# Performance work log

Hardware: AMD Instinct MI355X
Metric: run time of the kernel (lower is better)

## Reference

```python
import jax, jax.numpy as jnp
import numpy as np

NEG_INF = -1e9
LEAKY_SLOPE = 0.2


def setup_inputs() -> dict:
    key = jax.random.key(0)
    k1, k2, k3, k4, k5 = jax.random.split(key, 5)
    B, N, F_in, F_out = 8, 2048, 256, 256
    x = jax.random.normal(k1, (B, N, F_in), dtype=jnp.float32)
    adj = jax.random.randint(k2, (B, N, N), 0, 2, dtype=jnp.int32)
    W = jax.random.normal(k3, (F_out, F_in), dtype=jnp.float32) * 0.05
    a_src = jax.random.normal(k4, (F_out,), dtype=jnp.float32) * 0.05
    a_dst = jax.random.normal(k5, (F_out,), dtype=jnp.float32) * 0.05
    return {"x": x, "adj": adj, "W": W, "a_src": a_src, "a_dst": a_dst}


def reference(x, adj, W, a_src, a_dst):
    # h: (B, N, F_out)
    h = jnp.einsum("bnf,of->bno", x, W)
    # a([h_i ; h_j]) == h_i @ a_src + h_j @ a_dst  (avoids O(N^2, 2F) concat)
    s_src = h @ a_src  # (B, N) score contribution of row node i
    s_dst = h @ a_dst  # (B, N) score contribution of col node j
    e = s_src[:, :, None] + s_dst[:, None, :]  # (B, N, N)
    e = jax.nn.leaky_relu(e, negative_slope=LEAKY_SLOPE)
    e = jnp.where(adj == 0, jnp.float32(NEG_INF), e)
    alpha = jax.nn.softmax(e, axis=-1)  # dropout is identity in eval mode
    h_prime = jnp.einsum("bij,bjo->bio", alpha, h)
    return h_prime
```

## Files before the change

### kernel.cpp

```cpp
#include <hip/hip_runtime.h>
#include <hip/hip_bf16.h>
#include <cstdint>
#include <cstddef>

typedef __attribute__((ext_vector_type(8))) short short8;
typedef __attribute__((ext_vector_type(4))) short short4v;
typedef __attribute__((ext_vector_type(4))) float floatx4;
typedef unsigned short ushort_t;

#define LOG2E 1.44269504088896340736f

__device__ __forceinline__ unsigned short f2bf(float f) {
    unsigned u = __float_as_uint(f);
    u += 0x7FFFu + ((u >> 16) & 1u);
    return (unsigned short)(u >> 16);
}
__device__ __forceinline__ float bf2f(unsigned short s) {
    return __uint_as_float(((unsigned)s) << 16);
}

__global__ __launch_bounds__(256) void wprep(const float* __restrict__ W,
                                             ushort_t* __restrict__ Wb) {
    int t = blockIdx.x * 256 + threadIdx.x;
    float4 v = ((const float4*)W)[t];
    short4v s;
    s[0] = (short)f2bf(v.x); s[1] = (short)f2bf(v.y);
    s[2] = (short)f2bf(v.z); s[3] = (short)f2bf(v.w);
    ((short4v*)Wb)[t] = s;
}

__global__ __launch_bounds__(256) void gemm_h(const float* __restrict__ x,
                                              const ushort_t* __restrict__ Wb,
                                              ushort_t* __restrict__ hT,
                                              const float* __restrict__ a_src,
                                              const float* __restrict__ a_dst,
                                              float* __restrict__ s_src,
                                              float* __restrict__ s_dst) {
    const int tid = threadIdx.x;
    const int w = tid >> 6, lane = tid & 63;
    const int q = lane >> 4, t16 = lane & 15;

    __shared__ ushort_t wt[256][72];

    const int jrow = blockIdx.x * 64 + w * 16 + t16;
    const float* xr = x + (size_t)jrow * 256 + q * 8;
    short8 af[8];
#pragma unroll
    for (int kb = 0; kb < 8; ++kb) {
        float4 v0 = *(const float4*)(xr + kb * 32);
        float4 v1 = *(const float4*)(xr + kb * 32 + 4);
        short8 a;
        a[0] = (short)f2bf(v0.x); a[1] = (short)f2bf(v0.y);
        a[2] = (short)f2bf(v0.z); a[3] = (short)f2bf(v0.w);
        a[4] = (short)f2bf(v1.x); a[5] = (short)f2bf(v1.y);
        a[6] = (short)f2bf(v1.z); a[7] = (short)f2bf(v1.w);
        af[kb] = a;
    }

    floatx4 acc[16] = {};
#pragma unroll
    for (int kp = 0; kp < 4; ++kp) {
        if (kp) __syncthreads();
#pragma unroll
        for (int r = 0; r < 8; ++r) {
            int G = tid + 256 * r;
            int row = G >> 3, g = G & 7;
            int4 wv = *(const int4*)(Wb + (size_t)row * 256 + kp * 64 + g * 8);
            *(int4*)(&wt[row][g * 8]) = wv;
        }
        __syncthreads();
#pragma unroll
        for (int ks = 0; ks < 2; ++ks) {
#pragma unroll
            for (int ct = 0; ct < 16; ++ct) {
                short8 bf = *(const short8*)(&wt[ct * 16 + t16][ks * 32 + q * 8]);
                acc[ct] = __builtin_amdgcn_mfma_f32_16x16x32_bf16(af[kp * 2 + ks], bf, acc[ct], 0, 0, 0);
            }
        }
    }

    const int jbase = blockIdx.x * 64 + w * 16 + q * 4;
    const int b = jbase >> 11, jj = jbase & 2047;
#pragma unroll
    for (int ct = 0; ct < 16; ++ct) {
        const int o = ct * 16 + t16;
        short4v sv;
        sv[0] = (short)f2bf(acc[ct][0]);
        sv[1] = (short)f2bf(acc[ct][1]);
        sv[2] = (short)f2bf(acc[ct][2]);
        sv[3] = (short)f2bf(acc[ct][3]);
        *(short4v*)(hT + ((size_t)b * 256 + o) * 2048 + jj) = sv;
    }

    float psv[4] = {}, pdv[4] = {};
#pragma unroll
    for (int ct = 0; ct < 16; ++ct) {
        const int o = ct * 16 + t16;
        float as = a_src[o], ad = a_dst[o];
#pragma unroll
        for (int r = 0; r < 4; ++r) {
            psv[r] = __fmaf_rn(acc[ct][r], as, psv[r]);
            pdv[r] = __fmaf_rn(acc[ct][r], ad, pdv[r]);
        }
    }
#pragma unroll
    for (int m = 1; m < 16; m <<= 1) {
#pragma unroll
        for (int r = 0; r < 4; ++r) {
            psv[r] += __shfl_xor(psv[r], m);
            pdv[r] += __shfl_xor(pdv[r], m);
        }
    }
    if (t16 == 0) {
#pragma unroll
        for (int r = 0; r < 4; ++r) {
            s_src[jbase + r] = psv[r];
            s_dst[jbase + r] = pdv[r];
        }
    }
}

__global__ __launch_bounds__(256) void attn(const ushort_t* __restrict__ hT,
                                            const int* __restrict__ adj,
                                            const float* __restrict__ s_src,
                                            const float* __restrict__ s_dst,
                                            float* __restrict__ out) {
    const int tid = threadIdx.x;
    const int w = tid >> 6, lane = tid & 63;
    const int q = lane >> 4, t16 = lane & 15;
    const int b = blockIdx.x;
    const int i0 = blockIdx.y * 64;

    __shared__ ushort_t hts[2][256][40];
    __shared__ ushort_t ps[2][64][40];
    __shared__ float sdl[2048];
    __shared__ float lred[64][5];
    __shared__ float rll[64];

    const float* sdb = s_dst + (size_t)b * 2048;
#pragma unroll
    for (int k = 0; k < 2; ++k) {
        int idx = (k * 256 + tid) * 4;
        float4 v = *(const float4*)(sdb + idx);
        v.x *= LOG2E; v.y *= LOG2E; v.z *= LOG2E; v.w *= LOG2E;
        *(float4*)(&sdl[idx]) = v;
    }

    const int prow = tid & 63, jh = tid >> 6;
    const float si = s_src[(size_t)b * 2048 + i0 + prow] * LOG2E;
    const int* adjr = adj + ((size_t)b * 2048 + i0 + prow) * 2048 + jh * 8;
    const ushort_t* hTg = hT + ((size_t)b * 256 + tid) * 2048;

    const int osub = (w & 1) * 128, ih = (w >> 1) * 32;

    floatx4 acc[8][2] = {};
    float lsum = 0.f;
    int4 hreg[4];
    int4 a0, a1;

#pragma unroll
    for (int g = 0; g < 4; ++g)
        hreg[g] = *(const int4*)(hTg + g * 8);
    a0 = *(const int4*)(adjr);
    a1 = *(const int4*)(adjr + 4);
    __syncthreads();

    for (int c = 0; c < 64; ++c) {
        const int buf = c & 1;
#pragma unroll
        for (int g = 0; g < 4; ++g)
            *(int4*)(&hts[buf][tid][g * 8]) = hreg[g];
        {
            float4 s0 = *(const float4*)(&sdl[c * 32 + jh * 8]);
            float4 s1 = *(const float4*)(&sdl[c * 32 + jh * 8 + 4]);
            float sdv[8] = {s0.x, s0.y, s0.z, s0.w, s1.x, s1.y, s1.z, s1.w};
            int mv[8] = {a0.x, a0.y, a0.z, a0.w, a1.x, a1.y, a1.z, a1.w};
            short8 pv;
#pragma unroll
            for (int e = 0; e < 8; ++e) {
                float t = si + sdv[e];
                float lr = fmaxf(t, 0.2f * t);
                float pe = __builtin_amdgcn_exp2f(lr);
                pe = (mv[e] != 0) ? pe : 0.0f;
                unsigned short u = f2bf(pe);
                lsum += bf2f(u);
                pv[e] = (short)u;
            }
            *(short8*)(&ps[buf][prow][jh * 8]) = pv;
        }
        if (c < 63) {
#pragma unroll
            for (int g = 0; g < 4; ++g)
                hreg[g] = *(const int4*)(hTg + (c + 1) * 32 + g * 8);
            a0 = *(const int4*)(adjr + (c + 1) * 32);
            a1 = *(const int4*)(adjr + (c + 1) * 32 + 4);
        }
        __syncthreads();
        short8 bf0 = *(const short8*)(&ps[buf][ih + t16][q * 8]);
        short8 bf1 = *(const short8*)(&ps[buf][ih + 16 + t16][q * 8]);
#pragma unroll
        for (int ct = 0; ct < 8; ++ct) {
            short8 af = *(const short8*)(&hts[buf][osub + ct * 16 + t16][q * 8]);
            acc[ct][0] = __builtin_amdgcn_mfma_f32_16x16x32_bf16(af, bf0, acc[ct][0], 0, 0, 0);
            acc[ct][1] = __builtin_amdgcn_mfma_f32_16x16x32_bf16(af, bf1, acc[ct][1], 0, 0, 0);
        }
    }

    lred[prow][jh] = lsum;
    __syncthreads();
    if (tid < 64) {
        float s = lred[tid][0] + lred[tid][1] + lred[tid][2] + lred[tid][3];
        rll[tid] = (s > 0.f) ? 1.0f / s : 0.0f;
    }
    __syncthreads();

#pragma unroll
    for (int it = 0; it < 2; ++it) {
        const int i = ih + it * 16 + t16;
        const float rl = rll[i];
        float* orow = out + ((size_t)b * 2048 + i0 + i) * 256 + osub + q * 4;
#pragma unroll
        for (int ct = 0; ct < 8; ++ct) {
            floatx4 v = acc[ct][it] * rl;
            *(floatx4*)(orow + ct * 16) = v;
        }
    }
}

extern "C" void kernel_launch(void* const* d_in, const int* in_sizes, int n_in,
                              void* d_out, int out_size, void* d_ws, size_t ws_size,
                              hipStream_t stream) {
    const float* x     = (const float*)d_in[0];
    const int*   adj   = (const int*)d_in[1];
    const float* W     = (const float*)d_in[2];
    const float* a_src = (const float*)d_in[3];
    const float* a_dst = (const float*)d_in[4];
    float* out = (float*)d_out;

    char* ws = (char*)d_ws;
    ushort_t* hT = (ushort_t*)ws;
    float* s_src = (float*)(ws + (size_t)8 * 1024 * 1024);
    float* s_dst = s_src + 16384;
    ushort_t* Wb = (ushort_t*)(s_dst + 16384);

    wprep<<<64, 256, 0, stream>>>(W, Wb);
    gemm_h<<<256, 256, 0, stream>>>(x, Wb, hT, a_src, a_dst, s_src, s_dst);
    attn<<<dim3(8, 32), 256, 0, stream>>>(hT, adj, s_src, s_dst, out);
}
```

Before: 275.5 us.

## Widen attention blocks to 1024 threads, splitting work across 16 waves

The attention kernel now runs 1024 threads per block instead of 256, with the same 256-block grid. Each of the 16 waves computes a 16x64 output tile, and the per-thread adj, hT and probability work drops to two elements per chunk. The aim is more resident waves per CU to hide global memory latency on the adj stream, since 256 blocks at 4 waves left the GPU underoccupied. The cost is narrower 8-byte adj loads per thread, more barrier participants, and a 16-way row-sum reduction.

```diff
diff --git a/kernel.cpp b/kernel.cpp
--- a/kernel.cpp
+++ b/kernel.cpp
@@ -120,13 +120,14 @@
     }
 }
 
-__global__ __launch_bounds__(256) void attn(const ushort_t* __restrict__ hT,
-                                            const int* __restrict__ adj,
-                                            const float* __restrict__ s_src,
-                                            const float* __restrict__ s_dst,
-                                            float* __restrict__ out) {
+__global__ __launch_bounds__(1024) void attn(const ushort_t* __restrict__ hT,
+                                             const int* __restrict__ adj,
+                                             const float* __restrict__ s_src,
+                                             const float* __restrict__ s_dst,
+                                             float* __restrict__ out) {
     const int tid = threadIdx.x;
-    const int w = tid >> 6, lane = tid & 63;
+    const int w = tid >> 6;
+    const int lane = tid & 63;
     const int q = lane >> 4, t16 = lane & 15;
     const int b = blockIdx.x;
     const int i0 = blockIdx.y * 64;
@@ -134,94 +135,84 @@
     __shared__ ushort_t hts[2][256][40];
     __shared__ ushort_t ps[2][64][40];
     __shared__ float sdl[2048];
-    __shared__ float lred[64][5];
+    __shared__ float lred[64][16];
     __shared__ float rll[64];
 
     const float* sdb = s_dst + (size_t)b * 2048;
-#pragma unroll
-    for (int k = 0; k < 2; ++k) {
-        int idx = (k * 256 + tid) * 4;
-        float4 v = *(const float4*)(sdb + idx);
-        v.x *= LOG2E; v.y *= LOG2E; v.z *= LOG2E; v.w *= LOG2E;
-        *(float4*)(&sdl[idx]) = v;
-    }
-
-    const int prow = tid & 63, jh = tid >> 6;
+    {
+        int idx = tid * 2;
+        float2 v = *(const float2*)(sdb + idx);
+        v.x *= LOG2E; v.y *= LOG2E;
+        *(float2*)(&sdl[idx]) = v;
+    }
+
+    const int prow = lane;
     const float si = s_src[(size_t)b * 2048 + i0 + prow] * LOG2E;
-    const int* adjr = adj + ((size_t)b * 2048 + i0 + prow) * 2048 + jh * 8;
-    const ushort_t* hTg = hT + ((size_t)b * 256 + tid) * 2048;
-
-    const int osub = (w & 1) * 128, ih = (w >> 1) * 32;
-
-    floatx4 acc[8][2] = {};
+    const int* adjr = adj + ((size_t)b * 2048 + i0 + prow) * 2048 + w * 2;
+
+    const int hrow = tid >> 2, hseg = tid & 3;
+    const ushort_t* hTg = hT + ((size_t)b * 256 + hrow) * 2048 + hseg * 8;
+
+    const int osub = (w & 3) * 64, ih = (w >> 2) * 16;
+
+    floatx4 acc[4] = {};
     float lsum = 0.f;
-    int4 hreg[4];
-    int4 a0, a1;
-
-#pragma unroll
-    for (int g = 0; g < 4; ++g)
-        hreg[g] = *(const int4*)(hTg + g * 8);
-    a0 = *(const int4*)(adjr);
-    a1 = *(const int4*)(adjr + 4);
+    int4 hreg;
+    int2 a2;
+
+    hreg = *(const int4*)(hTg);
+    a2 = *(const int2*)(adjr);
     __syncthreads();
 
     for (int c = 0; c < 64; ++c) {
         const int buf = c & 1;
-#pragma unroll
-        for (int g = 0; g < 4; ++g)
-            *(int4*)(&hts[buf][tid][g * 8]) = hreg[g];
+        *(int4*)(&hts[buf][hrow][hseg * 8]) = hreg;
         {
-            float4 s0 = *(const float4*)(&sdl[c * 32 + jh * 8]);
-            float4 s1 = *(const float4*)(&sdl[c * 32 + jh * 8 + 4]);
-            float sdv[8] = {s0.x, s0.y, s0.z, s0.w, s1.x, s1.y, s1.z, s1.w};
-            int mv[8] = {a0.x, a0.y, a0.z, a0.w, a1.x, a1.y, a1.z, a1.w};
-            short8 pv;
-#pragma unroll
-            for (int e = 0; e < 8; ++e) {
-                float t = si + sdv[e];
-                float lr = fmaxf(t, 0.2f * t);
-                float pe = __builtin_amdgcn_exp2f(lr);
-                pe = (mv[e] != 0) ? pe : 0.0f;
-                unsigned short u = f2bf(pe);
-                lsum += bf2f(u);
-                pv[e] = (short)u;
-            }
-            *(short8*)(&ps[buf][prow][jh * 8]) = pv;
+            float2 sd = *(const float2*)(&sdl[c * 32 + w * 2]);
+            float t0 = si + sd.x;
+            float t1 = si + sd.y;
+            float l0 = fmaxf(t0, 0.2f * t0);
+            float l1 = fmaxf(t1, 0.2f * t1);
+            float p0 = __builtin_amdgcn_exp2f(l0);
+            float p1 = __builtin_amdgcn_exp2f(l1);
+            p0 = (a2.x != 0) ? p0 : 0.0f;
+            p1 = (a2.y != 0) ? p1 : 0.0f;
+            unsigned short u0 = f2bf(p0);
+            unsigned short u1 = f2bf(p1);
+            lsum += bf2f(u0) + bf2f(u1);
+            unsigned pw = (unsigned)u0 | ((unsigned)u1 << 16);
+            *(unsigned*)(&ps[buf][prow][w * 2]) = pw;
         }
         if (c < 63) {
-#pragma unroll
-            for (int g = 0; g < 4; ++g)
-                hreg[g] = *(const int4*)(hTg + (c + 1) * 32 + g * 8);
-            a0 = *(const int4*)(adjr + (c + 1) * 32);
-            a1 = *(const int4*)(adjr + (c + 1) * 32 + 4);
+            hreg = *(const int4*)(hTg + (c + 1) * 32);
+            a2 = *(const int2*)(adjr + (size_t)(c + 1) * 32);
         }
         __syncthreads();
-        short8 bf0 = *(const short8*)(&ps[buf][ih + t16][q * 8]);
-        short8 bf1 = *(const short8*)(&ps[buf][ih + 16 + t16][q * 8]);
-#pragma unroll
-        for (int ct = 0; ct < 8; ++ct) {
+        short8 bf = *(const short8*)(&ps[buf][ih + t16][q * 8]);
+#pragma unroll
+        for (int ct = 0; ct < 4; ++ct) {
             short8 af = *(const short8*)(&hts[buf][osub + ct * 16 + t16][q * 8]);
-            acc[ct][0] = __builtin_amdgcn_mfma_f32_16x16x32_bf16(af, bf0, acc[ct][0], 0, 0, 0);
-            acc[ct][1] = __builtin_amdgcn_mfma_f32_16x16x32_bf16(af, bf1, acc[ct][1], 0, 0, 0);
-        }
-    }
-
-    lred[prow][jh] = lsum;
+            acc[ct] = __builtin_amdgcn_mfma_f32_16x16x32_bf16(af, bf, acc[ct], 0, 0, 0);
+        }
+    }
+
+    lred[prow][w] = lsum;
     __syncthreads();
     if (tid < 64) {
-        float s = lred[tid][0] + lred[tid][1] + lred[tid][2] + lred[tid][3];
+        float s = 0.f;
+#pragma unroll
+        for (int k = 0; k < 16; ++k) s += lred[tid][k];
         rll[tid] = (s > 0.f) ? 1.0f / s : 0.0f;
     }
     __syncthreads();
 
-#pragma unroll
-    for (int it = 0; it < 2; ++it) {
-        const int i = ih + it * 16 + t16;
+    {
+        const int i = ih + t16;
         const float rl = rll[i];
         float* orow = out + ((size_t)b * 2048 + i0 + i) * 256 + osub + q * 4;
 #pragma unroll
-        for (int ct = 0; ct < 8; ++ct) {
-            floatx4 v = acc[ct][it] * rl;
+        for (int ct = 0; ct < 4; ++ct) {
+            floatx4 v = acc[ct] * rl;
             *(floatx4*)(orow + ct * 16) = v;
         }
     }
@@ -245,5 +236,5 @@
 
     wprep<<<64, 256, 0, stream>>>(W, Wb);
     gemm_h<<<256, 256, 0, stream>>>(x, Wb, hT, a_src, a_dst, s_src, s_dst);
-    attn<<<dim3(8, 32), 256, 0, stream>>>(hT, adj, s_src, s_dst, out);
-}
+    attn<<<dim3(8, 32), 1024, 0, stream>>>(hT, adj, s_src, s_dst, out);
+}
```

Result: faster. 246.9 us (-10.4%).
